# Optimization experiments

Measured on AMD Instinct MI355X. Metric: run time of the kernel, lower is better.

## Reference

```python
import jax, jax.numpy as jnp
import numpy as np

B, N, D = 4, 512, 64
EPS = 1e-5          # nn.LayerNorm default
NEG_SLOPE = 0.01    # nn.LeakyReLU default


def setup_inputs() -> dict:
    key = jax.random.key(0)
    k1, k2, k3 = jax.random.split(key, 3)
    i_em = jax.random.normal(k1, (B, N, D), dtype=jnp.float32)
    # att_a: Linear(2*D -> 1); store weight as flat (2*D,) plus scalar bias
    W_a = jax.random.normal(k2, (2 * D,), dtype=jnp.float32) * 0.05
    b_a = jax.random.normal(k3, (1,), dtype=jnp.float32) * 0.05
    gamma = jnp.ones((D,), dtype=jnp.float32)
    beta = jnp.zeros((D,), dtype=jnp.float32)
    return {"i_em": i_em, "W_a": W_a, "b_a": b_a, "gamma": gamma, "beta": beta}


def reference(i_em, W_a, b_a, gamma, beta):
    # LayerNorm over last dim
    mu = jnp.mean(i_em, axis=-1, keepdims=True)
    var = jnp.mean(jnp.square(i_em - mu), axis=-1, keepdims=True)
    xn = (i_em - mu) * jax.lax.rsqrt(var + EPS) * gamma + beta  # [B,N,D]

    # Fused additive attention: cat(q,k) @ W == q @ W[:D] + k @ W[D:]
    a_q, a_k = W_a[:D], W_a[D:]
    sq = jnp.einsum("bnd,d->bn", xn, a_q)          # query contribution
    sk = jnp.einsum("bnd,d->bn", xn, a_k)          # key contribution
    scores = sq[:, :, None] + sk[:, None, :] + b_a[0]  # [B,N,N]
    scores = jnp.where(scores >= 0, scores, NEG_SLOPE * scores)  # LeakyReLU
    # dropout is identity in eval mode
    alphas = jax.nn.softmax(scores, axis=-1)[..., None]  # [B,N,N,1]

    # elementwise outer product on the UN-normalized embeddings
    value = i_em[:, :, None, :] * i_em[:, None, :, :]  # [B,N,N,D]
    return (alphas, value)
```

## Files before the change

### kernel.cpp

```cpp
#include <hip/hip_runtime.h>
#include <math.h>

#define BB 4
#define NN 512
#define DD 64
#define EPS 1e-5f
#define NEG_SLOPE 0.01f

__global__ void __launch_bounds__(256)
stats_kernel(const float* __restrict__ i_em,
             const float* __restrict__ W_a,
             const float* __restrict__ gamma,
             const float* __restrict__ beta,
             float* __restrict__ sq,
             float* __restrict__ sk) {
    int row  = (blockIdx.x * blockDim.x + threadIdx.x) >> 6;
    int lane = threadIdx.x & 63;
    if (row >= BB * NN) return;

    float x = i_em[row * DD + lane];

    float s = x;
    #pragma unroll
    for (int off = 32; off >= 1; off >>= 1) s += __shfl_xor(s, off, 64);
    float mu = s * (1.0f / DD);

    float dx = x - mu;
    float v = dx * dx;
    #pragma unroll
    for (int off = 32; off >= 1; off >>= 1) v += __shfl_xor(v, off, 64);
    float rstd = rsqrtf(v * (1.0f / DD) + EPS);

    float xn = dx * rstd * gamma[lane] + beta[lane];
    float pq = xn * W_a[lane];
    float pk = xn * W_a[DD + lane];
    #pragma unroll
    for (int off = 32; off >= 1; off >>= 1) {
        pq += __shfl_xor(pq, off, 64);
        pk += __shfl_xor(pk, off, 64);
    }
    if (lane == 0) { sq[row] = pq; sk[row] = pk; }
}

__global__ void __launch_bounds__(256)
attn_kernel(const float* __restrict__ i_em,
            const float* __restrict__ sq,
            const float* __restrict__ sk,
            const float* __restrict__ b_a,
            float* __restrict__ alphas,
            float* __restrict__ value) {
    __shared__ float red[4];

    const int blk = blockIdx.x;
    const int b   = blk >> 9;
    const int t   = threadIdx.x;

    const float bias = b_a[0];
    const float si   = sq[blk];

    float s0 = si + sk[b * NN + t]       + bias;
    s0 = (s0 >= 0.f) ? s0 : NEG_SLOPE * s0;
    float s1 = si + sk[b * NN + t + 256] + bias;
    s1 = (s1 >= 0.f) ? s1 : NEG_SLOPE * s1;

    float m = fmaxf(s0, s1);
    #pragma unroll
    for (int off = 32; off >= 1; off >>= 1) m = fmaxf(m, __shfl_xor(m, off, 64));
    const int w = t >> 6;
    if ((t & 63) == 0) red[w] = m;
    __syncthreads();
    m = fmaxf(fmaxf(red[0], red[1]), fmaxf(red[2], red[3]));
    __syncthreads();

    float e0 = expf(s0 - m);
    float e1 = expf(s1 - m);
    float sum = e0 + e1;
    #pragma unroll
    for (int off = 32; off >= 1; off >>= 1) sum += __shfl_xor(sum, off, 64);
    if ((t & 63) == 0) red[w] = sum;
    __syncthreads();
    sum = red[0] + red[1] + red[2] + red[3];
    const float inv = 1.0f / sum;

    alphas[blk * NN + t]       = e0 * inv;
    alphas[blk * NN + t + 256] = e1 * inv;

    const float4* em4 = (const float4*)i_em;
    const int d4 = t & 15;
    const int jg = t >> 4;
    const float4 xi = em4[blk * 16 + d4];
    const float4* emb = em4 + (size_t)b * NN * 16;
    float4* out4 = (float4*)value + (size_t)blk * (NN * 16);

    #pragma unroll 4
    for (int j = jg; j < NN; j += 16) {
        float4 xj = emb[j * 16 + d4];
        float4 o;
        o.x = xi.x * xj.x;
        o.y = xi.y * xj.y;
        o.z = xi.z * xj.z;
        o.w = xi.w * xj.w;
        out4[j * 16 + d4] = o;
    }
}

extern "C" void kernel_launch(void* const* d_in, const int* in_sizes, int n_in,
                              void* d_out, int out_size, void* d_ws, size_t ws_size,
                              hipStream_t stream) {
    const float* i_em  = (const float*)d_in[0];
    const float* W_a   = (const float*)d_in[1];
    const float* b_a   = (const float*)d_in[2];
    const float* gamma = (const float*)d_in[3];
    const float* beta  = (const float*)d_in[4];

    float* alphas = (float*)d_out;
    float* value  = (float*)d_out + (size_t)BB * NN * NN;

    float* sq = (float*)d_ws;
    float* sk = sq + BB * NN;

    stats_kernel<<<(BB * NN) / 4, 256, 0, stream>>>(i_em, W_a, gamma, beta, sq, sk);
    attn_kernel<<<BB * NN, 256, 0, stream>>>(i_em, sq, sk, b_a, alphas, value);
}
```

Before: 272.1 us.

## Process four query rows per block with per-wave softmax and nontemporal stores

Each block now handles four query rows instead of one. Each wavefront computes one row's softmax entirely with shuffles, so the shared-memory reductions and __syncthreads are gone. The outer-product loop reuses each loaded key embedding across four rows and writes the large value output with nontemporal stores to avoid polluting cache. The trade-off is fewer blocks (512) and more registers per thread, which could lower occupancy on a store-bandwidth-bound write of about 268MB.

Result: slower. 281.8 us (+3.6%).

```diff
diff --git a/kernel.cpp b/kernel.cpp
--- a/kernel.cpp
+++ b/kernel.cpp
@@ -6,6 +6,9 @@
 #define DD 64
 #define EPS 1e-5f
 #define NEG_SLOPE 0.01f
+#define TI 4
+
+typedef float f32x4 __attribute__((ext_vector_type(4)));
 
 __global__ void __launch_bounds__(256)
 stats_kernel(const float* __restrict__ i_em,
@@ -49,58 +52,65 @@
             const float* __restrict__ b_a,
             float* __restrict__ alphas,
             float* __restrict__ value) {
-    __shared__ float red[4];
-
-    const int blk = blockIdx.x;
-    const int b   = blk >> 9;
-    const int t   = threadIdx.x;
+    const int blk  = blockIdx.x;
+    const int i0g  = blk * TI;
+    const int b    = i0g >> 9;
+    const int t    = threadIdx.x;
+    const int lane = t & 63;
+    const int w    = t >> 6;
 
     const float bias = b_a[0];
-    const float si   = sq[blk];
 
-    float s0 = si + sk[b * NN + t]       + bias;
-    s0 = (s0 >= 0.f) ? s0 : NEG_SLOPE * s0;
-    float s1 = si + sk[b * NN + t + 256] + bias;
-    s1 = (s1 >= 0.f) ? s1 : NEG_SLOPE * s1;
+    {
+        const int row  = i0g + w;
+        const float si = sq[row] + bias;
+        const float* skb = sk + b * NN;
 
-    float m = fmaxf(s0, s1);
-    #pragma unroll
-    for (int off = 32; off >= 1; off >>= 1) m = fmaxf(m, __shfl_xor(m, off, 64));
-    const int w = t >> 6;
-    if ((t & 63) == 0) red[w] = m;
-    __syncthreads();
-    m = fmaxf(fmaxf(red[0], red[1]), fmaxf(red[2], red[3]));
-    __syncthreads();
+        float e[8];
+        float m = -INFINITY;
+        #pragma unroll
+        for (int k = 0; k < 8; ++k) {
+            float s = si + skb[lane + k * 64];
+            s = (s >= 0.f) ? s : NEG_SLOPE * s;
+            e[k] = s;
+            m = fmaxf(m, s);
+        }
+        #pragma unroll
+        for (int off = 32; off >= 1; off >>= 1) m = fmaxf(m, __shfl_xor(m, off, 64));
 
-    float e0 = expf(s0 - m);
-    float e1 = expf(s1 - m);
-    float sum = e0 + e1;
-    #pragma unroll
-    for (int off = 32; off >= 1; off >>= 1) sum += __shfl_xor(sum, off, 64);
-    if ((t & 63) == 0) red[w] = sum;
-    __syncthreads();
-    sum = red[0] + red[1] + red[2] + red[3];
-    const float inv = 1.0f / sum;
+        float sum = 0.f;
+        #pragma unroll
+        for (int k = 0; k < 8; ++k) { e[k] = expf(e[k] - m); sum += e[k]; }
+        #pragma unroll
+        for (int off = 32; off >= 1; off >>= 1) sum += __shfl_xor(sum, off, 64);
+        const float inv = 1.0f / sum;
 
-    alphas[blk * NN + t]       = e0 * inv;
-    alphas[blk * NN + t + 256] = e1 * inv;
+        float* arow = alphas + (size_t)row * NN;
+        #pragma unroll
+        for (int k = 0; k < 8; ++k)
+            __builtin_nontemporal_store(e[k] * inv, &arow[lane + k * 64]);
+    }
 
-    const float4* em4 = (const float4*)i_em;
+    const f32x4* em4 = (const f32x4*)i_em;
     const int d4 = t & 15;
     const int jg = t >> 4;
-    const float4 xi = em4[blk * 16 + d4];
-    const float4* emb = em4 + (size_t)b * NN * 16;
-    float4* out4 = (float4*)value + (size_t)blk * (NN * 16);
+    const f32x4* emb = em4 + (size_t)b * NN * 16;
+
+    f32x4 xi[TI];
+    #pragma unroll
+    for (int r = 0; r < TI; ++r) xi[r] = em4[(size_t)(i0g + r) * 16 + d4];
+
+    f32x4* out0 = (f32x4*)value + (size_t)i0g * (NN * 16) + d4;
 
     #pragma unroll 4
-    for (int j = jg; j < NN; j += 16) {
-        float4 xj = emb[j * 16 + d4];
-        float4 o;
-        o.x = xi.x * xj.x;
-        o.y = xi.y * xj.y;
-        o.z = xi.z * xj.z;
-        o.w = xi.w * xj.w;
-        out4[j * 16 + d4] = o;
+    for (int k = 0; k < NN / 16; ++k) {
+        const int j = jg + k * 16;
+        const f32x4 xj = emb[j * 16 + d4];
+        #pragma unroll
+        for (int r = 0; r < TI; ++r) {
+            f32x4 o = xi[r] * xj;
+            __builtin_nontemporal_store(o, out0 + (size_t)r * (NN * 16) + j * 16);
+        }
     }
 }
 
@@ -120,5 +130,5 @@
     float* sk = sq + BB * NN;
 
     stats_kernel<<<(BB * NN) / 4, 256, 0, stream>>>(i_em, W_a, gamma, beta, sq, sk);
-    attn_kernel<<<BB * NN, 256, 0, stream>>>(i_em, sq, sk, b_a, alphas, value);
+    attn_kernel<<<(BB * NN) / TI, 256, 0, stream>>>(i_em, sq, sk, b_a, alphas, value);
 }
```
